# Kernel tuning notes

Hardware: AMD Instinct MI355X
Metric: run time of the kernel (lower is better)

Reference implementation:

```python
import jax, jax.numpy as jnp
import numpy as np
from jax import lax

EPS = 1e-12  # torch F.normalize eps
DN = ('NCHW', 'OIHW', 'NCHW')


def setup_inputs() -> dict:
    B, C, H, W, K = 16, 64, 192, 192, 3
    key = jax.random.key(0)
    k1, k2, k3 = jax.random.split(key, 3)
    x = jax.random.normal(k1, (B, C, H, W), dtype=jnp.float32)
    # Conv2d(n_feat, 2*n_feat, 3, stride=3, bias=False) weight
    w_qk = jax.random.normal(k2, (2 * C, C, 3, 3), dtype=jnp.float32) * np.float32(np.sqrt(1.0 / (C * 9)))
    # Parameter(C,C,K,K), kaiming_normal_ (fan_in=C*K*K, gain=sqrt(2)) then *0.1
    std = np.float32(np.sqrt(2.0 / (C * K * K)) * 0.1)
    weight = jax.random.normal(k3, (C, C, K, K), dtype=jnp.float32) * std
    # temperature Parameter (1,1,1); init zeros in the module, use 0.5 so the
    # dynamic-kernel branch is exercised numerically
    temperature = jnp.full((1, 1, 1), 0.5, dtype=jnp.float32)
    return {"x": x, "w_qk": w_qk, "weight": weight, "temperature": temperature}


def _l2_normalize_per_sample(t):
    # t: (B, ...) -> L2-normalize flattened per sample (torch F.normalize)
    n = jnp.sqrt(jnp.sum(t.reshape(t.shape[0], -1) ** 2, axis=-1))
    n = jnp.maximum(n, EPS).reshape((t.shape[0],) + (1,) * (t.ndim - 1))
    return t / n


def reference(x, w_qk, weight, temperature):
    B, C, H, W = x.shape
    K = weight.shape[-1]
    S = 2 * K - 1  # 5: number of spatial shifts in the cross-covariance
    P = K - 1

    # qk conv: stride-3 valid conv -> (B, 2C, H2, W2)
    qk = lax.conv_general_dilated(x, w_qk, (3, 3), 'VALID', dimension_numbers=DN)
    q, k = jnp.split(qk, 2, axis=1)
    q = _l2_normalize_per_sample(q)
    k = _l2_normalize_per_sample(k)
    H2, W2 = q.shape[2], q.shape[3]

    # cal_xtx: attn[b, co, ci, i, j] = sum_{h,w} q_pad[b, ci, i+h, j+w] * k[b, co, h, w]
    q_pad = jnp.pad(q, ((0, 0), (0, 0), (P, P), (P, P)))
    rows = []
    for i in range(S):  # fixed small 5x5 shift set
        row = []
        for j in range(S):
            sl = lax.dynamic_slice(q_pad, (0, 0, i, j), (B, C, H2, W2))
            row.append(jnp.einsum('bchw,bdhw->bdc', sl, k))  # (B, co, ci)
        rows.append(jnp.stack(row, axis=-1))
    attn = jnp.stack(rows, axis=-2)  # (B, C, C, S, S)

    # conv2d(attn.view(B*C, C, S, S), weight) valid -> (B*C, C, K, K)
    ak = lax.conv_general_dilated(attn.reshape(B * C, C, S, S), weight, (1, 1), 'VALID', dimension_numbers=DN)
    ak = ak.reshape(B, C, C, K, K).transpose(0, 2, 1, 3, 4)  # swap the two C dims

    # normalize each (C,K,K) slice per (b, c0)
    n = jnp.sqrt(jnp.sum(ak.reshape(B, C, -1) ** 2, axis=-1))
    ak = ak / jnp.maximum(n, EPS)[:, :, None, None, None]

    kern = weight[None] + ak * temperature  # (B, C, C, K, K)

    # sample-wise conv2d: groups=B trick
    out = lax.conv_general_dilated(
        x.reshape(1, B * C, H, W), kern.reshape(B * C, C, K, K), (1, 1),
        [(K // 2, K // 2)] * 2, dimension_numbers=DN, feature_group_count=B)
    return jax.nn.relu(out.reshape(B, C, H, W))
```

## Files before the change

### kernel.cpp

```cpp
#include <hip/hip_runtime.h>
#include <cstddef>

#define BB 16
#define CC_ 64
#define HH 192
#define WW 192
#define HW2 4096
#define XPH 194
#define XPW 196

typedef _Float16 f16x8 __attribute__((ext_vector_type(8)));
typedef float f32x4 __attribute__((ext_vector_type(4)));

__global__ __launch_bounds__(1024) void k_wpack(const float* __restrict__ wqk,
                                                _Float16* __restrict__ wh) {
  int e = blockIdx.x * 1024 + threadIdx.x;
  int co = e / 576, t = e % 576;
  int ci = t / 9, rs = t % 9;
  int r = rs / 3, s = rs % 3;
  int ch = ci >> 5, t32 = ci & 31;
  wh[(((r * 2 + ch) * 128 + co) * 96) + s * 32 + t32] = (_Float16)wqk[e];
}

__global__ __launch_bounds__(256) void k_xhalo(_Float16* __restrict__ xh) {
  int e = blockIdx.x * 256 + threadIdx.x;
  int b = e / 9280, i = e % 9280;
  int r, px, c;
  if (i < 3136) {
    r = (i < 1568) ? 0 : 193;
    int j = (i < 1568) ? i : i - 1568;
    px = j >> 3;
    c = j & 7;
  } else {
    int i2 = i - 3136;
    r = 1 + (i2 >> 5);
    int rem = i2 & 31;
    int sel = rem >> 3;
    px = (sel == 0) ? 0 : 192 + sel;
    c = rem & 7;
  }
  *(f16x8*)(xh + (((size_t)b * XPH + r) * XPW + px) * 64 + c * 8) =
      (f16x8)(_Float16)0;
}

__global__ __launch_bounds__(256) void k_xpack(const float* __restrict__ x,
                                               _Float16* __restrict__ xh) {
  int blk = blockIdx.x;
  int xg = blk % 3;
  int t = blk / 3;
  int y = t % 192, b = t / 192;
  int x0 = xg * 64;
  __shared__ _Float16 tl[64 * 72];
  int tid = threadIdx.x;
  int ci = tid >> 2, c4 = (tid & 3) * 16;
  const float* xp = x + ((size_t)(b * 64 + ci) * HH + y) * WW + x0 + c4;
#pragma unroll
  for (int i = 0; i < 4; ++i) {
    float4 v = *(const float4*)(xp + i * 4);
    tl[(c4 + i * 4 + 0) * 72 + ci] = (_Float16)v.x;
    tl[(c4 + i * 4 + 1) * 72 + ci] = (_Float16)v.y;
    tl[(c4 + i * 4 + 2) * 72 + ci] = (_Float16)v.z;
    tl[(c4 + i * 4 + 3) * 72 + ci] = (_Float16)v.w;
  }
  __syncthreads();
#pragma unroll
  for (int i = 0; i < 2; ++i) {
    int e = tid + 256 * i;
    int col = e >> 3, g = e & 7;
    *(f16x8*)(xh + (((size_t)b * XPH + y + 1) * XPW + x0 + 1 + col) * 64 + g * 8) =
        *(f16x8*)&tl[col * 72 + g * 8];
  }
}

__global__ __launch_bounds__(256) void k_qkconv(const _Float16* __restrict__ xh,
                                                const _Float16* __restrict__ wh,
                                                _Float16* __restrict__ qkh) {
  int blk = blockIdx.x;
  int pt = blk & 31, b = blk >> 5;
  int tid = threadIdx.x;
  int w = tid >> 6, lane = tid & 63, n16 = lane & 15, quad = lane >> 4;
  int mh = w & 1, nh = w >> 1;
  const _Float16* xb = xh + (size_t)b * (XPH * XPW * 64);

  f32x4 acc[4][4];
#pragma unroll
  for (int mt = 0; mt < 4; ++mt)
#pragma unroll
    for (int nt = 0; nt < 4; ++nt) acc[mt][nt] = (f32x4){0.f, 0.f, 0.f, 0.f};

#pragma unroll
  for (int kc = 0; kc < 6; ++kc) {
    int r = kc >> 1, ch = kc & 1;
    int irow = 6 * pt + 3 * nh + r;
    const _Float16* wp = wh + (size_t)kc * (128 * 96);
#pragma unroll
    for (int s = 0; s < 3; ++s) {
      f16x8 af[4], bf[4];
#pragma unroll
      for (int mt = 0; mt < 4; ++mt)
        af[mt] = *(const f16x8*)(wp + (mh * 64 + mt * 16 + n16) * 96 + s * 32 +
                                 quad * 8);
#pragma unroll
      for (int nt = 0; nt < 4; ++nt) {
        int col = 3 * (nt * 16 + n16) + s;
        bf[nt] = *(const f16x8*)(xb + ((size_t)(irow + 1) * XPW + col + 1) * 64 +
                                 ch * 32 + quad * 8);
      }
#pragma unroll
      for (int mt = 0; mt < 4; ++mt)
#pragma unroll
        for (int nt = 0; nt < 4; ++nt)
          acc[mt][nt] = __builtin_amdgcn_mfma_f32_16x16x32_f16(af[mt], bf[nt],
                                                               acc[mt][nt], 0, 0, 0);
    }
  }
  int py = pt * 2 + nh;
#pragma unroll
  for (int mt = 0; mt < 4; ++mt)
#pragma unroll
    for (int reg = 0; reg < 4; ++reg) {
      int co = mh * 64 + mt * 16 + quad * 4 + reg;
      _Float16* op = qkh + (size_t)(b * 128 + co) * HW2 + py * 64;
#pragma unroll
      for (int nt = 0; nt < 4; ++nt) op[nt * 16 + n16] = (_Float16)acc[mt][nt][reg];
    }
}

__global__ __launch_bounds__(256) void k_qpad(const _Float16* __restrict__ qkh,
                                              _Float16* __restrict__ qpad) {
  int blk = blockIdx.x;
  int b = blk >> 6, ci = blk & 63;
  __shared__ _Float16 qrow[4096];
  int tid = threadIdx.x;
  const _Float16* src = qkh + (size_t)(b * 128 + ci) * HW2;
#pragma unroll
  for (int i = 0; i < 2; ++i)
    ((f16x8*)qrow)[tid + 256 * i] = ((const f16x8*)src)[tid + 256 * i];
  __syncthreads();
  _Float16* dst = qpad + ((size_t)(b * 5) * 64 + ci) * 4352;
  const f16x8 zero = (f16x8)(_Float16)0;
  for (int it = tid; it < 544; it += 256) {
    int w8 = it & 7, hr = it >> 3;
    int h = hr - 2;
    bool rowok = (unsigned)h < 64u;
    f16x8 vm = (rowok && w8 > 0) ? *(const f16x8*)&qrow[h * 64 + w8 * 8 - 8] : zero;
    f16x8 vc = rowok ? *(const f16x8*)&qrow[h * 64 + w8 * 8] : zero;
    f16x8 vp = (rowok && w8 < 7) ? *(const f16x8*)&qrow[h * 64 + w8 * 8 + 8] : zero;
#pragma unroll
    for (int djx = 0; djx < 5; ++djx) {
      const int s = djx - 2;
      f16x8 r;
#pragma unroll
      for (int j = 0; j < 8; ++j) {
        const int rel = j + s;
        r[j] = (rel < 0) ? vm[8 + rel] : ((rel < 8) ? vc[rel] : vp[rel - 8]);
      }
      *(f16x8*)(dst + (size_t)djx * (64 * 4352) + hr * 64 + w8 * 8) = r;
    }
  }
}

__global__ __launch_bounds__(256) void k_attn(const _Float16* __restrict__ qkh,
                                              const _Float16* __restrict__ qpad,
                                              float* __restrict__ attn_p) {
  int blk = blockIdx.x;
  int xcd = blk & 7, j = blk >> 3;
  int b = xcd + ((j >= 100) ? 8 : 0);
  int t = (j >= 100) ? (j - 100) : j;
  int sh = t >> 2, sp = t & 3;
  int djx = sh % 5, dix = sh / 5;
  int tid = threadIdx.x, w = tid >> 6, lane = tid & 63;
  int n16 = lane & 15, quad = lane >> 4;

  const _Float16* ka = qkh + (size_t)(b * 128 + 64 + w * 16 + n16) * HW2 +
                       sp * 1024 + quad * 8;
  const _Float16* qa = qpad + ((size_t)(b * 5 + djx) * 64 + n16) * 4352 +
                       dix * 64 + sp * 1024 + quad * 8;

  f32x4 acc[4];
#pragma unroll
  for (int nt = 0; nt < 4; ++nt) acc[nt] = (f32x4){0.f, 0.f, 0.f, 0.f};

  f16x8 afA, bfA[4], afB, bfB[4];
  afA = *(const f16x8*)ka;
#pragma unroll
  for (int nt = 0; nt < 4; ++nt)
    bfA[nt] = *(const f16x8*)(qa + (size_t)nt * 69632);

#pragma unroll
  for (int ks = 0; ks < 32; ks += 2) {
    afB = *(const f16x8*)(ka + (ks + 1) * 32);
#pragma unroll
    for (int nt = 0; nt < 4; ++nt)
      bfB[nt] = *(const f16x8*)(qa + (size_t)nt * 69632 + (ks + 1) * 32);
#pragma unroll
    for (int nt = 0; nt < 4; ++nt)
      acc[nt] = __builtin_amdgcn_mfma_f32_16x16x32_f16(afA, bfA[nt], acc[nt],
                                                       0, 0, 0);
    if (ks + 2 < 32) {
      afA = *(const f16x8*)(ka + (ks + 2) * 32);
#pragma unroll
      for (int nt = 0; nt < 4; ++nt)
        bfA[nt] = *(const f16x8*)(qa + (size_t)nt * 69632 + (ks + 2) * 32);
    }
#pragma unroll
    for (int nt = 0; nt < 4; ++nt)
      acc[nt] = __builtin_amdgcn_mfma_f32_16x16x32_f16(afB, bfB[nt], acc[nt],
                                                       0, 0, 0);
  }

  float* op = attn_p + (size_t)(b * 25 + sh) * 4096;
#pragma unroll
  for (int nt = 0; nt < 4; ++nt)
#pragma unroll
    for (int reg = 0; reg < 4; ++reg) {
      int co = w * 16 + quad * 4 + reg;
      atomicAdd(&op[co * 64 + nt * 16 + n16], acc[nt][reg]);
    }
}

__global__ __launch_bounds__(576) void k_akconv(const float* __restrict__ attn_p,
                                                const float* __restrict__ wgt,
                                                float* __restrict__ akt) {
  int blk = blockIdx.x;
  int b = blk >> 6, co = blk & 63;
  __shared__ float sa[64 * 25];
  int tid = threadIdx.x;
  for (int e = tid; e < 1600; e += 576) {
    int didj = e >> 6, ci = e & 63;
    size_t idx = (((size_t)b * 25 + didj) * 64 + co) * 64 + ci;
    sa[ci * 25 + didj] = attn_p[idx];
  }
  __syncthreads();
  int o = tid / 9, rs = tid % 9;
  int ki = rs / 3, kj = rs % 3;
  float acc = 0.f;
  for (int ci = 0; ci < 64; ++ci) {
    const float* wp = wgt + (o * 64 + ci) * 9;
    const float* ap = sa + ci * 25 + ki * 5 + kj;
#pragma unroll
    for (int r = 0; r < 3; ++r)
#pragma unroll
      for (int s = 0; s < 3; ++s) acc += ap[r * 5 + s] * wp[r * 3 + s];
  }
  akt[((size_t)(b * 64 + o) * 64 + co) * 9 + rs] = acc;
}

__global__ __launch_bounds__(576) void k_kern(const float* __restrict__ akt,
                                              const float* __restrict__ wgt,
                                              const float* __restrict__ temp,
                                              _Float16* __restrict__ kh) {
  int blk = blockIdx.x;
  int o = blk & 63;
  int tid = threadIdx.x;
  float v = akt[(size_t)blk * 576 + tid];
  float sq = v * v;
#pragma unroll
  for (int m = 1; m < 64; m <<= 1) sq += __shfl_xor(sq, m, 64);
  __shared__ float wsum[9];
  if ((tid & 63) == 0) wsum[tid >> 6] = sq;
  __syncthreads();
  float tot = 0.f;
#pragma unroll
  for (int i = 0; i < 9; ++i) tot += wsum[i];
  float inv = temp[0] / fmaxf(sqrtf(tot), 1e-12f);
  float kv = wgt[o * 576 + tid] + v * inv;
  int b = blk >> 6;
  int ci = tid / 9, rs = tid % 9;
  kh[(((size_t)(b * 9 + rs) * 64 + o) * 64) + ci] = (_Float16)kv;
}

__global__ __launch_bounds__(256, 3) void k_final(const _Float16* __restrict__ xh,
                                                  const _Float16* __restrict__ kh,
                                                  float* __restrict__ out) {
  int blk = blockIdx.x;
  int xt = blk % 3;
  int t2 = blk / 3;
  int yt = t2 % 48, b = t2 / 48;
  int y0 = yt * 4, x0 = xt * 64;

  __shared__ __align__(16) _Float16 xs[6 * 68 * 64];

  int tid = threadIdx.x;
  int w = tid >> 6, lane = tid & 63;
  int n16 = lane & 15, quad = lane >> 4;

  const _Float16* xb = xh + (size_t)b * (XPH * XPW * 64);
  const _Float16* kb = kh + (size_t)b * (9 * 64 * 64);

  {
    f16x8 v[13];
#pragma unroll
    for (int i = 0; i < 13; ++i) {
      int e = tid + 256 * i;
      if (e < 3264) {
        int row = e / 544, rem = e % 544;
        int px = rem >> 3, c = rem & 7;
        v[i] = *(const f16x8*)(xb + ((size_t)(y0 + row) * XPW + x0 + px) * 64 +
                               c * 8);
      }
    }
#pragma unroll
    for (int i = 0; i < 13; ++i) {
      int e = tid + 256 * i;
      if (e < 3264) {
        int row = e / 544, rem = e % 544;
        int px = rem >> 3, c = rem & 7;
        *(f16x8*)&xs[((row * 68 + px) * 8 + (c ^ (px & 7))) * 8] = v[i];
      }
    }
  }
  __syncthreads();

  f32x4 acc[4][4];
#pragma unroll
  for (int mt = 0; mt < 4; ++mt)
#pragma unroll
    for (int nt = 0; nt < 4; ++nt) acc[mt][nt] = (f32x4){0.f, 0.f, 0.f, 0.f};

#define LDAF(dst, ch_)                                                          \
  {                                                                             \
    const int rs_ = (ch_) >> 1, hi_ = (ch_)&1;                                  \
    _Pragma("unroll") for (int mt = 0; mt < 4; ++mt) dst[mt] =                  \
        *(const f16x8*)(kb + ((size_t)rs_ * 64 + mt * 16 + n16) * 64 +          \
                        hi_ * 32 + quad * 8);                                   \
  }

  f16x8 af[3][4];
  LDAF(af[0], 0)
  LDAF(af[1], 1)

#pragma unroll
  for (int ch = 0; ch < 18; ++ch) {
    if (ch + 2 < 18) LDAF(af[(ch + 2) % 3], ch + 2)
    int rs = ch >> 1, hi = ch & 1;
    int r = rs / 3, s = rs % 3;
    int trow = w + r;
    f16x8 bf[4];
#pragma unroll
    for (int nt = 0; nt < 4; ++nt) {
      int px = nt * 16 + n16 + s;
      int c = (hi * 4 + quad) ^ (px & 7);
      bf[nt] = *(const f16x8*)&xs[((trow * 68 + px) * 8 + c) * 8];
    }
#pragma unroll
    for (int mt = 0; mt < 4; ++mt)
#pragma unroll
      for (int nt = 0; nt < 4; ++nt)
        acc[mt][nt] = __builtin_amdgcn_mfma_f32_16x16x32_f16(af[ch % 3][mt],
                                                             bf[nt], acc[mt][nt],
                                                             0, 0, 0);
  }
#undef LDAF

  int y = y0 + w;
#pragma unroll
  for (int mt = 0; mt < 4; ++mt)
#pragma unroll
    for (int reg = 0; reg < 4; ++reg) {
      int o = mt * 16 + quad * 4 + reg;
      float* op = out + (((size_t)(b * 64 + o) * HH + y) * WW + x0);
#pragma unroll
      for (int nt = 0; nt < 4; ++nt)
        op[nt * 16 + n16] = fmaxf(acc[mt][nt][reg], 0.f);
    }
}

extern "C" void kernel_launch(void* const* d_in, const int* in_sizes, int n_in,
                              void* d_out, int out_size, void* d_ws, size_t ws_size,
                              hipStream_t stream) {
  const float* x = (const float*)d_in[0];
  const float* wqk = (const float*)d_in[1];
  const float* wgt = (const float*)d_in[2];
  const float* temp = (const float*)d_in[3];
  float* out = (float*)d_out;
  char* ws = (char*)d_ws;

  _Float16* xh = (_Float16*)ws;
  _Float16* qkh = (_Float16*)(ws + 77873152);
  _Float16* qpad = (_Float16*)(ws + 94650368);
  float* attn_p = (float*)(ws + 139214848);
  _Float16* wh = (_Float16*)(ws + 139067392);
  float* akt = (float*)(ws + 94650368);
  _Float16* kh = (_Float16*)(ws + 97009664);

  hipMemsetAsync(attn_p, 0, 6553600, stream);
  k_wpack<<<dim3(72), 1024, 0, stream>>>(wqk, wh);
  k_xhalo<<<dim3(580), 256, 0, stream>>>(xh);
  k_xpack<<<dim3(9216), 256, 0, stream>>>(x, xh);
  k_qkconv<<<dim3(512), 256, 0, stream>>>(xh, wh, qkh);
  k_qpad<<<dim3(1024), 256, 0, stream>>>(qkh, qpad);
  k_attn<<<dim3(1600), 256, 0, stream>>>(qkh, qpad, attn_p);
  k_akconv<<<dim3(1024), 576, 0, stream>>>(attn_p, wgt, akt);
  k_kern<<<dim3(1024), 576, 0, stream>>>(akt, wgt, temp, kh);
  k_final<<<dim3(2304), 256, 0, stream>>>(xh, kh, out);
}
```

Before: 591.1 us.

## Replace split-K atomics in attn kernel with in-block LDS reduction

The attention cross-covariance kernel now gives each block the whole K range of one (batch, shift) pair. Two wave halves each cover half of K and combine their partial sums through shared memory before a plain store. This removes the global atomicAdd accumulation and the memset of the output buffer, and deepens the register prefetch to four slots. The cost is 4x fewer blocks (400 of 512 threads), which lowers parallelism on a 256-CU device and raises register pressure.

```diff
diff --git a/kernel.cpp b/kernel.cpp
--- a/kernel.cpp
+++ b/kernel.cpp
@@ -160,63 +160,67 @@
   }
 }
 
-__global__ __launch_bounds__(256) void k_attn(const _Float16* __restrict__ qkh,
+__global__ __launch_bounds__(512) void k_attn(const _Float16* __restrict__ qkh,
                                               const _Float16* __restrict__ qpad,
                                               float* __restrict__ attn_p) {
   int blk = blockIdx.x;
   int xcd = blk & 7, j = blk >> 3;
-  int b = xcd + ((j >= 100) ? 8 : 0);
-  int t = (j >= 100) ? (j - 100) : j;
-  int sh = t >> 2, sp = t & 3;
+  int b = xcd + ((j >= 25) ? 8 : 0);
+  int sh = (j >= 25) ? (j - 25) : j;
   int djx = sh % 5, dix = sh / 5;
   int tid = threadIdx.x, w = tid >> 6, lane = tid & 63;
   int n16 = lane & 15, quad = lane >> 4;
-
-  const _Float16* ka = qkh + (size_t)(b * 128 + 64 + w * 16 + n16) * HW2 +
-                       sp * 1024 + quad * 8;
+  int g = w >> 1, h = w & 1;
+
+  __shared__ float lpart[4096];
+
+  const _Float16* ka = qkh + (size_t)(b * 128 + 64 + g * 16 + n16) * HW2 +
+                       h * 2048 + quad * 8;
   const _Float16* qa = qpad + ((size_t)(b * 5 + djx) * 64 + n16) * 4352 +
-                       dix * 64 + sp * 1024 + quad * 8;
+                       dix * 64 + h * 2048 + quad * 8;
 
   f32x4 acc[4];
 #pragma unroll
   for (int nt = 0; nt < 4; ++nt) acc[nt] = (f32x4){0.f, 0.f, 0.f, 0.f};
 
-  f16x8 afA, bfA[4], afB, bfB[4];
-  afA = *(const f16x8*)ka;
-#pragma unroll
-  for (int nt = 0; nt < 4; ++nt)
-    bfA[nt] = *(const f16x8*)(qa + (size_t)nt * 69632);
-
-#pragma unroll
-  for (int ks = 0; ks < 32; ks += 2) {
-    afB = *(const f16x8*)(ka + (ks + 1) * 32);
+  f16x8 afS[4], bfS[4][4];
+#define LDSLOT(sl, k_)                                                         \
+  {                                                                            \
+    afS[sl] = *(const f16x8*)(ka + (k_)*32);                                   \
+    _Pragma("unroll") for (int nt = 0; nt < 4; ++nt) bfS[sl][nt] =             \
+        *(const f16x8*)(qa + (size_t)nt * 69632 + (k_)*32);                    \
+  }
+  LDSLOT(0, 0) LDSLOT(1, 1) LDSLOT(2, 2) LDSLOT(3, 3)
+
+#pragma unroll
+  for (int ks = 0; ks < 64; ++ks) {
+    const int sl = ks & 3;
 #pragma unroll
     for (int nt = 0; nt < 4; ++nt)
-      bfB[nt] = *(const f16x8*)(qa + (size_t)nt * 69632 + (ks + 1) * 32);
+      acc[nt] = __builtin_amdgcn_mfma_f32_16x16x32_f16(afS[sl], bfS[sl][nt],
+                                                       acc[nt], 0, 0, 0);
+    if (ks + 4 < 64) LDSLOT(sl, ks + 4)
+  }
+#undef LDSLOT
+
+  if (h == 0) {
 #pragma unroll
     for (int nt = 0; nt < 4; ++nt)
-      acc[nt] = __builtin_amdgcn_mfma_f32_16x16x32_f16(afA, bfA[nt], acc[nt],
-                                                       0, 0, 0);
-    if (ks + 2 < 32) {
-      afA = *(const f16x8*)(ka + (ks + 2) * 32);
-#pragma unroll
-      for (int nt = 0; nt < 4; ++nt)
-        bfA[nt] = *(const f16x8*)(qa + (size_t)nt * 69632 + (ks + 2) * 32);
-    }
+#pragma unroll
+      for (int reg = 0; reg < 4; ++reg)
+        lpart[(g * 16 + quad * 4 + reg) * 64 + nt * 16 + n16] = acc[nt][reg];
+  }
+  __syncthreads();
+  if (h == 1) {
+    float* op = attn_p + (size_t)(b * 25 + sh) * 4096;
 #pragma unroll
     for (int nt = 0; nt < 4; ++nt)
-      acc[nt] = __builtin_amdgcn_mfma_f32_16x16x32_f16(afB, bfB[nt], acc[nt],
-                                                       0, 0, 0);
-  }
-
-  float* op = attn_p + (size_t)(b * 25 + sh) * 4096;
-#pragma unroll
-  for (int nt = 0; nt < 4; ++nt)
-#pragma unroll
-    for (int reg = 0; reg < 4; ++reg) {
-      int co = w * 16 + quad * 4 + reg;
-      atomicAdd(&op[co * 64 + nt * 16 + n16], acc[nt][reg]);
-    }
+#pragma unroll
+      for (int reg = 0; reg < 4; ++reg) {
+        int idx = (g * 16 + quad * 4 + reg) * 64 + nt * 16 + n16;
+        op[idx] = lpart[idx] + acc[nt][reg];
+      }
+  }
 }
 
 __global__ __launch_bounds__(576) void k_akconv(const float* __restrict__ attn_p,
@@ -384,13 +388,12 @@
   float* akt = (float*)(ws + 94650368);
   _Float16* kh = (_Float16*)(ws + 97009664);
 
-  hipMemsetAsync(attn_p, 0, 6553600, stream);
   k_wpack<<<dim3(72), 1024, 0, stream>>>(wqk, wh);
   k_xhalo<<<dim3(580), 256, 0, stream>>>(xh);
   k_xpack<<<dim3(9216), 256, 0, stream>>>(x, xh);
   k_qkconv<<<dim3(512), 256, 0, stream>>>(xh, wh, qkh);
   k_qpad<<<dim3(1024), 256, 0, stream>>>(qkh, qpad);
-  k_attn<<<dim3(1600), 256, 0, stream>>>(qkh, qpad, attn_p);
+  k_attn<<<dim3(400), 512, 0, stream>>>(qkh, qpad, attn_p);
   k_akconv<<<dim3(1024), 576, 0, stream>>>(attn_p, wgt, akt);
   k_kern<<<dim3(1024), 576, 0, stream>>>(akt, wgt, temp, kh);
   k_final<<<dim3(2304), 256, 0, stream>>>(xh, kh, out);
```

After: 598.8 us. Within noise of the previous version (+1.3%).
